# Optimization experiments

Measured on AMD Instinct MI355X. Metric: run time of the kernel, lower is better.

Reference implementation:

```python
import jax, jax.numpy as jnp
import numpy as np

ACTION_FEAT_DIM = 64
ACTION_EMB = 192
FUSION = 768
HID = 384
N_HEADS = 4
B, A = 2048, 64

gelu = lambda x: jax.nn.gelu(x, approximate=False)


def setup_inputs() -> dict:
    key = jax.random.key(0)
    ks = jax.random.split(key, 12)
    s = lambda fan_in: 1.0 / np.sqrt(fan_in)
    in_dim = ACTION_EMB + FUSION
    return {
        "action_feats": jax.random.normal(ks[0], (B, A, ACTION_FEAT_DIM), jnp.float32),
        "action_mask": jax.random.bernoulli(ks[1], 0.5, (B, A)),
        "fused": jax.random.normal(ks[2], (B, FUSION), jnp.float32),
        "phase_oh": jax.random.normal(ks[3], (B, 5), jnp.float32),
        # action encoder: Linear(64->192), GELU, Linear(192->192), GELU
        "We1": jax.random.uniform(ks[4], (ACTION_FEAT_DIM, ACTION_EMB), jnp.float32, -s(ACTION_FEAT_DIM), s(ACTION_FEAT_DIM)),
        "be1": jnp.zeros((ACTION_EMB,), jnp.float32),
        "We2": jax.random.uniform(ks[5], (ACTION_EMB, ACTION_EMB), jnp.float32, -s(ACTION_EMB), s(ACTION_EMB)),
        "be2": jnp.zeros((ACTION_EMB,), jnp.float32),
        # 4 phase heads: Linear(960->384), GELU, Linear(384->1), stacked on leading head axis
        "W1": jax.random.uniform(ks[6], (N_HEADS, in_dim, HID), jnp.float32, -s(in_dim), s(in_dim)),
        "b1": jnp.zeros((N_HEADS, HID), jnp.float32),
        "W2": jax.random.uniform(ks[7], (N_HEADS, HID), jnp.float32, -s(HID), s(HID)),
        "b2": jnp.zeros((N_HEADS,), jnp.float32),
    }


def reference(action_feats, action_mask, fused, phase_oh, We1, be1, We2, be2, W1, b1, W2, b2):
    bsz, act_count, _ = action_feats.shape
    # action encoder
    emb = gelu(gelu(action_feats @ We1 + be1) @ We2 + be2)          # [B,A,192]
    fused_rep = jnp.broadcast_to(fused[:, None, :], (bsz, act_count, fused.shape[-1]))
    inp = jnp.concatenate([emb, fused_rep], axis=-1)                 # [B,A,960]
    # dense compute of all 4 heads (faithful to original)
    h = gelu(jnp.einsum('bai,kio->bkao', inp, W1) + b1[None, :, None, :])  # [B,4,A,384]
    per_head = jnp.einsum('bkao,ko->bka', h, W2) + b2[None, :, None]       # [B,4,A]
    # phase routing: argmax over one-hot, phases >=3 map to head 3
    phase_idx = jnp.argmax(phase_oh, axis=-1)
    head_idx = jnp.where(phase_idx <= 2, phase_idx, 3)               # [B]
    logits = jnp.take_along_axis(per_head, head_idx[:, None, None], axis=1)[:, 0, :]  # [B,A]
    return jnp.where(action_mask, jnp.float32(-10000.0), logits)
```

## Files before the change

### kernel.cpp

```cpp
#include <hip/hip_runtime.h>


typedef __bf16 bf16x8 __attribute__((ext_vector_type(8)));
typedef unsigned short ushortx8 __attribute__((ext_vector_type(8)));
typedef float floatx4 __attribute__((ext_vector_type(4)));
typedef unsigned short u16;
typedef unsigned int u32;

#define B_SZ 2048
#define EMB 192
#define FUS 768
#define HID 384
#define INDIM 960
#define LDS_W 200

#define WS_FLAGS 0
#define WS_CNT 64
#define WS_HEAD 256
#define WS_LIST 8448
#define WS_W1T 41216
#define WS_WE1T 2990336
#define WS_WE2T 3014912
#define WS_FUSEDBF 3088640
#define WS_GSEL 6234368

__device__ __forceinline__ float bf2f(u16 u) {
  return __uint_as_float(((u32)u) << 16);
}
__device__ __forceinline__ u16 f2bf(float f) {
  u32 x = __float_as_uint(f);
  x += 0x7FFFu + ((x >> 16) & 1u);
  return (u16)(x >> 16);
}
__device__ __forceinline__ float ldf(const void* p, size_t i, int bf) {
  return bf ? bf2f(((const u16*)p)[i]) : ((const float*)p)[i];
}
__device__ __forceinline__ bf16x8 ld8(const void* p, size_t idx, int bf) {
  if (bf) return *reinterpret_cast<const bf16x8*>((const u16*)p + idx);
  const float* f = (const float*)p + idx;
  ushortx8 u;
#pragma unroll
  for (int i = 0; i < 8; ++i) u[i] = f2bf(f[i]);
  return __builtin_bit_cast(bf16x8, u);
}

__device__ __forceinline__ float gelu_f(float x) {
  float t = __expf(-1.702f * x);
  return x * __builtin_amdgcn_rcpf(1.0f + t);
}

__device__ __forceinline__ bool read_mask(const void* m, long long i, int fmt) {
  if (fmt == 0) return ((const int*)m)[i] != 0;
  if (fmt == 1) return ((const unsigned char*)m)[i] != 0;
  if (fmt == 2) return ((const u16*)m)[i] != 0;
  return ((const u32*)m)[i] != 0;
}

__global__ void k_detect(const u32* __restrict__ aw, int* __restrict__ flags,
                         int* __restrict__ cnt) {
  __shared__ u32 so[4];
  __shared__ int sc[4];
  int tid = threadIdx.x;
  int lane = tid & 63, wave = tid >> 6;
  u32 orv = 0;
  int c = 0;
#pragma unroll 8
  for (int j = 0; j < 64; ++j) {
    u32 w = aw[j * 256 + tid];
    u32 h = w & 0xFFFFu;
    orv |= h;
    u32 e = (h >> 7) & 0xFFu;
    c += (h == 0u || (e >= 90u && e <= 150u)) ? 1 : 0;
  }
#pragma unroll
  for (int off = 32; off >= 1; off >>= 1) {
    orv |= (u32)__shfl_xor((int)orv, off);
    c += __shfl_xor(c, off);
  }
  if (lane == 0) { so[wave] = orv; sc[wave] = c; }
  __syncthreads();
  if (tid == 0) {
    u32 o = so[0] | so[1] | so[2] | so[3];
    int ct = sc[0] + sc[1] + sc[2] + sc[3];
    flags[3] = (o != 0u && ct > 12288) ? 1 : 0;
    flags[0] = 0; flags[1] = 0; flags[2] = 0;
    cnt[0] = 0; cnt[1] = 0; cnt[2] = 0; cnt[3] = 0;
  }
}

__global__ void k_prep(const void* __restrict__ fused, u16* __restrict__ fbf,
                       const int* __restrict__ flags) {
  const int bf = flags[3];
  int gid = blockIdx.x * 256 + threadIdx.x;
  if (bf) {
    const uint2* s = (const uint2*)fused;
    uint2* d = (uint2*)fbf;
    for (int i = gid; i < 393216; i += 49152) d[i] = s[i];
  } else {
    const float4* s = (const float4*)fused;
    uint2* d = (uint2*)fbf;
    for (int i = gid; i < 393216; i += 49152) {
      float4 v = s[i];
      uint2 o;
      o.x = (u32)f2bf(v.x) | ((u32)f2bf(v.y) << 16);
      o.y = (u32)f2bf(v.z) | ((u32)f2bf(v.w) << 16);
      d[i] = o;
    }
  }
}

__global__ void k_route(const void* __restrict__ phase, const void* __restrict__ mask,
                        int* __restrict__ head_idx, int* __restrict__ flags,
                        int* __restrict__ cnt, int* __restrict__ list) {
  int tid = threadIdx.x;
  int t = blockIdx.x * 256 + tid;
  const int bf = flags[3];
  float best = ldf(phase, (size_t)t * 5, bf);
  int bi = 0;
#pragma unroll
  for (int i = 1; i < 5; ++i) {
    float v = ldf(phase, (size_t)t * 5 + i, bf);
    if (v > best) { best = v; bi = i; }
  }
  int h = (bi <= 2) ? bi : 3;
  head_idx[t] = h;
  int pos = atomicAdd(&cnt[h], 1);
  list[h * 2048 + pos] = t;

  const u32* mw = (const u32*)mask;
  u32 vi = 0, vu = 0, en = 0;
#pragma unroll
  for (int j = 0; j < 16; ++j) {
    u32 w = mw[blockIdx.x * 4096 + j * 256 + tid];
    vi |= (u32)(w > 1u);
    vu |= (u32)((w & 0xFEFEFEFEu) != 0u);
    en |= (u32)((w & 0x0000FFFFu) != 0u);
  }
  if (vi) atomicOr(&flags[0], 1);
  if (vu) atomicOr(&flags[1], 1);
  if (en) atomicOr(&flags[2], 1);
}

__global__ void k_transpose(const void* __restrict__ we1, const void* __restrict__ we2,
                            const void* __restrict__ w1, u16* __restrict__ we1t,
                            u16* __restrict__ we2t, u16* __restrict__ w1t,
                            const int* __restrict__ flags) {
  __shared__ u16 tile[32][33];
  const int bf = flags[3];
  const void* src; u16* dst; int R, C; size_t soff = 0;
  int z = blockIdx.z;
  if (z == 0)      { src = we1; dst = we1t; R = 64;  C = EMB; }
  else if (z == 1) { src = we2; dst = we2t; R = EMB; C = EMB; }
  else { src = w1; soff = (size_t)(z - 2) * INDIM * HID;
         dst = w1t + (size_t)(z - 2) * HID * INDIM; R = INDIM; C = HID; }
  int bx = blockIdx.x, by = blockIdx.y;
  if (bx * 32 >= C || by * 32 >= R) return;
  int tx = threadIdx.x, ty = threadIdx.y;
#pragma unroll
  for (int i = 0; i < 4; ++i) {
    int r = by * 32 + ty + i * 8, c = bx * 32 + tx;
    if (r < R && c < C) tile[ty + i * 8][tx] = f2bf(ldf(src, soff + (size_t)r * C + c, bf));
  }
  __syncthreads();
#pragma unroll
  for (int i = 0; i < 4; ++i) {
    int r = bx * 32 + ty + i * 8, c = by * 32 + tx;
    if (r < C && c < R) dst[(size_t)r * R + c] = tile[tx][ty + i * 8];
  }
}

__global__ __launch_bounds__(256, 4) void k_gall_sel(
    const u16* __restrict__ fbf, const u16* __restrict__ w1t,
    const void* __restrict__ b1, u16* __restrict__ gsel,
    const int* __restrict__ cnt, const int* __restrict__ list,
    const int* __restrict__ flags) {
  const int bf = flags[3];
  int c0 = cnt[0], c1 = cnt[1], c2 = cnt[2], c3 = cnt[3];
  int t0 = (c0 + 63) >> 6, t1 = (c1 + 63) >> 6, t2 = (c2 + 63) >> 6, t3 = (c3 + 63) >> 6;
  int x = blockIdx.x, h, tl;
  if (x < t0) { h = 0; tl = x; }
  else if (x < t0 + t1) { h = 1; tl = x - t0; }
  else if (x < t0 + t1 + t2) { h = 2; tl = x - t0 - t1; }
  else if (x < t0 + t1 + t2 + t3) { h = 3; tl = x - t0 - t1 - t2; }
  else return;
  int ch = (h == 0) ? c0 : (h == 1) ? c1 : (h == 2) ? c2 : c3;
  const int tid = threadIdx.x;
  const int w = tid >> 6, lane = tid & 63;
  const int nl = lane & 15, q = lane >> 4;

  int r = tl * 64 + w * 16 + nl;
  if (r >= ch) r = ch - 1;
  int bi = list[h * 2048 + r];
  const u16* arow = fbf + (size_t)bi * FUS;
  const u16* w1h = w1t + (size_t)h * HID * INDIM;
  const int ncol0 = blockIdx.y * 64;

  const floatx4 z4 = {0.f, 0.f, 0.f, 0.f};
  floatx4 acc[4];
#pragma unroll
  for (int i = 0; i < 4; ++i) acc[i] = z4;
#pragma unroll 4
  for (int kk = 0; kk < 24; ++kk) {
    bf16x8 a = *reinterpret_cast<const bf16x8*>(arow + kk * 32 + q * 8);
#pragma unroll
    for (int nt = 0; nt < 4; ++nt) {
      int col = ncol0 + nt * 16 + nl;
      bf16x8 bb = *reinterpret_cast<const bf16x8*>(w1h + (size_t)col * INDIM + EMB + kk * 32 + q * 8);
      acc[nt] = __builtin_amdgcn_mfma_f32_16x16x32_bf16(a, bb, acc[nt], 0, 0, 0);
    }
  }
  int bi2[4];
#pragma unroll
  for (int rr = 0; rr < 4; ++rr) {
    int rm = tl * 64 + w * 16 + q * 4 + rr;
    if (rm >= ch) rm = ch - 1;
    bi2[rr] = list[h * 2048 + rm];
  }
#pragma unroll
  for (int nt = 0; nt < 4; ++nt) {
    int col = ncol0 + nt * 16 + nl;
    float bias = ldf(b1, (size_t)h * HID + col, bf);
#pragma unroll
    for (int rr = 0; rr < 4; ++rr)
      gsel[(size_t)bi2[rr] * HID + col] = f2bf(acc[nt][rr] + bias);
  }
}

__global__ __launch_bounds__(256, 4) void k_main(
    const void* __restrict__ act, const void* __restrict__ mask,
    const void* __restrict__ be1, const void* __restrict__ be2,
    const void* __restrict__ W2, const void* __restrict__ b2,
    const u16* __restrict__ we1t, const u16* __restrict__ we2t,
    const u16* __restrict__ w1t, const u16* __restrict__ gsel,
    const int* __restrict__ head_idx, const int* __restrict__ flags,
    void* __restrict__ out) {
  __shared__ __align__(16) u16 S[64 * LDS_W];
  __shared__ float red[256];
  const int b = blockIdx.x;
  const int tid = threadIdx.x;
  const int w = tid >> 6, lane = tid & 63;
  const int nl = lane & 15, q = lane >> 4;
  const int khead = head_idx[b];
  const int bf = flags[3];
  const floatx4 z4 = {0.f, 0.f, 0.f, 0.f};

  {
    floatx4 acc1[4][3];
#pragma unroll
    for (int mt = 0; mt < 4; ++mt)
#pragma unroll
      for (int nt = 0; nt < 3; ++nt) acc1[mt][nt] = z4;
#pragma unroll
    for (int kk = 0; kk < 2; ++kk) {
      bf16x8 a[4];
#pragma unroll
      for (int mt = 0; mt < 4; ++mt)
        a[mt] = ld8(act, ((size_t)b * 64 + mt * 16 + nl) * 64 + kk * 32 + q * 8, bf);
#pragma unroll
      for (int nt = 0; nt < 3; ++nt) {
        bf16x8 bb = *reinterpret_cast<const bf16x8*>(we1t + (w * 48 + nt * 16 + nl) * 64 + kk * 32 + q * 8);
#pragma unroll
        for (int mt = 0; mt < 4; ++mt)
          acc1[mt][nt] = __builtin_amdgcn_mfma_f32_16x16x32_bf16(a[mt], bb, acc1[mt][nt], 0, 0, 0);
      }
    }
#pragma unroll
    for (int nt = 0; nt < 3; ++nt) {
      int col = w * 48 + nt * 16 + nl;
      float bias = ldf(be1, col, bf);
#pragma unroll
      for (int mt = 0; mt < 4; ++mt)
#pragma unroll
        for (int r = 0; r < 4; ++r)
          S[(mt * 16 + q * 4 + r) * LDS_W + col] = f2bf(gelu_f(acc1[mt][nt][r] + bias));
    }
  }
  __syncthreads();

  {
    floatx4 acc2[4][3];
#pragma unroll
    for (int mt = 0; mt < 4; ++mt)
#pragma unroll
      for (int nt = 0; nt < 3; ++nt) acc2[mt][nt] = z4;
#pragma unroll
    for (int kk = 0; kk < 6; ++kk) {
      bf16x8 a[4];
#pragma unroll
      for (int mt = 0; mt < 4; ++mt)
        a[mt] = *reinterpret_cast<const bf16x8*>(&S[(mt * 16 + nl) * LDS_W + kk * 32 + q * 8]);
#pragma unroll
      for (int nt = 0; nt < 3; ++nt) {
        bf16x8 bb = *reinterpret_cast<const bf16x8*>(we2t + (w * 48 + nt * 16 + nl) * EMB + kk * 32 + q * 8);
#pragma unroll
        for (int mt = 0; mt < 4; ++mt)
          acc2[mt][nt] = __builtin_amdgcn_mfma_f32_16x16x32_bf16(a[mt], bb, acc2[mt][nt], 0, 0, 0);
      }
    }
    __syncthreads();
#pragma unroll
    for (int nt = 0; nt < 3; ++nt) {
      int col = w * 48 + nt * 16 + nl;
      float bias = ldf(be2, col, bf);
#pragma unroll
      for (int mt = 0; mt < 4; ++mt)
#pragma unroll
        for (int r = 0; r < 4; ++r)
          S[(mt * 16 + q * 4 + r) * LDS_W + col] = f2bf(gelu_f(acc2[mt][nt][r] + bias));
    }
  }
  __syncthreads();

  float partial[4][4];
#pragma unroll
  for (int mt = 0; mt < 4; ++mt)
#pragma unroll
    for (int r = 0; r < 4; ++r) partial[mt][r] = 0.f;
  const u16* w1h = w1t + (size_t)khead * HID * INDIM;
  const u16* grow = gsel + (size_t)b * HID;
#pragma unroll
  for (int half = 0; half < 2; ++half) {
    floatx4 acc3[4][3];
#pragma unroll
    for (int mt = 0; mt < 4; ++mt)
#pragma unroll
      for (int nt = 0; nt < 3; ++nt) acc3[mt][nt] = z4;
#pragma unroll
    for (int kk = 0; kk < 6; ++kk) {
      bf16x8 a[4];
#pragma unroll
      for (int mt = 0; mt < 4; ++mt)
        a[mt] = *reinterpret_cast<const bf16x8*>(&S[(mt * 16 + nl) * LDS_W + kk * 32 + q * 8]);
#pragma unroll
      for (int nt = 0; nt < 3; ++nt) {
        int col = w * 96 + half * 48 + nt * 16 + nl;
        bf16x8 bb = *reinterpret_cast<const bf16x8*>(w1h + (size_t)col * INDIM + kk * 32 + q * 8);
#pragma unroll
        for (int mt = 0; mt < 4; ++mt)
          acc3[mt][nt] = __builtin_amdgcn_mfma_f32_16x16x32_bf16(a[mt], bb, acc3[mt][nt], 0, 0, 0);
      }
    }
#pragma unroll
    for (int nt = 0; nt < 3; ++nt) {
      int col = w * 96 + half * 48 + nt * 16 + nl;
      float g = bf2f(grow[col]);
      float w2c = ldf(W2, (size_t)khead * HID + col, bf);
#pragma unroll
      for (int mt = 0; mt < 4; ++mt)
#pragma unroll
        for (int r = 0; r < 4; ++r)
          partial[mt][r] += gelu_f(acc3[mt][nt][r] + g) * w2c;
    }
  }
#pragma unroll
  for (int off = 1; off < 16; off <<= 1)
#pragma unroll
    for (int mt = 0; mt < 4; ++mt)
#pragma unroll
      for (int r = 0; r < 4; ++r)
        partial[mt][r] += __shfl_xor(partial[mt][r], off, 16);
  if (nl == 0) {
#pragma unroll
    for (int mt = 0; mt < 4; ++mt)
#pragma unroll
      for (int r = 0; r < 4; ++r)
        red[w * 64 + mt * 16 + q * 4 + r] = partial[mt][r];
  }
  __syncthreads();

  if (tid < 64) {
    float s = red[tid] + red[64 + tid] + red[128 + tid] + red[192 + tid];
    int f0 = flags[0], f1 = flags[1], f2v = flags[2];
    int fmt = (f0 == 0) ? 0 : ((f1 == 0) ? 1 : ((f2v != 0) ? 2 : 3));
    float bb2 = ldf(b2, khead, bf);
    long long mi = (long long)b * 64 + tid;
    float v = read_mask(mask, mi, fmt) ? -10000.0f : (s + bb2);
    if (bf) ((u16*)out)[mi] = f2bf(v);
    else    ((float*)out)[mi] = v;
  }
}

extern "C" void kernel_launch(void* const* d_in, const int* in_sizes, int n_in,
                              void* d_out, int out_size, void* d_ws, size_t ws_size,
                              hipStream_t stream) {
  const void* act   = d_in[0];
  const void* mask  = d_in[1];
  const void* fused = d_in[2];
  const void* phase = d_in[3];
  const void* We1 = d_in[4];
  const void* be1 = d_in[5];
  const void* We2 = d_in[6];
  const void* be2 = d_in[7];
  const void* W1  = d_in[8];
  const void* b1  = d_in[9];
  const void* W2  = d_in[10];
  const void* b2  = d_in[11];
  char* ws = (char*)d_ws;
  int* flags    = (int*)(ws + WS_FLAGS);
  int* cnt      = (int*)(ws + WS_CNT);
  int* head_idx = (int*)(ws + WS_HEAD);
  int* list     = (int*)(ws + WS_LIST);
  u16* w1t  = (u16*)(ws + WS_W1T);
  u16* we1t = (u16*)(ws + WS_WE1T);
  u16* we2t = (u16*)(ws + WS_WE2T);
  u16* fbf  = (u16*)(ws + WS_FUSEDBF);
  u16* gsel = (u16*)(ws + WS_GSEL);

  k_detect<<<1, 256, 0, stream>>>((const u32*)act, flags, cnt);
  k_route<<<8, 256, 0, stream>>>(phase, mask, head_idx, flags, cnt, list);
  k_prep<<<192, 256, 0, stream>>>(fused, fbf, flags);
  k_transpose<<<dim3(12, 30, 6), dim3(32, 8), 0, stream>>>(We1, We2, W1, we1t, we2t, w1t, flags);
  k_gall_sel<<<dim3(36, 6), 256, 0, stream>>>(fbf, w1t, b1, gsel, cnt, list, flags);
  k_main<<<B_SZ, 256, 0, stream>>>(act, mask, be1, be2, W2, b2, we1t, we2t,
                                   w1t, gsel, head_idx, flags, d_out);
}
```

Baseline: 226.8 us.

## Process two head-sorted batch rows per block and merge prep kernels

The main kernel now handles two batch rows per block, picked from the per-head sorted lists so both rows tend to share a head. This doubles the M dimension of the encoder GEMMs so each encoder weight fragment is reused across twice as many rows, and it improves locality for the W1 head weights. The detect kernel is folded into routing, with a cheaper dtype check that samples only 64 words. The fused-input conversion is merged into the transpose kernel, and flags and counters are cleared with a memset, which cuts the number of launches. In exchange, shared memory and register use double and launch bounds drop to 2 blocks per CU, which may hurt latency hiding.

```diff
diff --git a/kernel.cpp b/kernel.cpp
--- a/kernel.cpp
+++ b/kernel.cpp
@@ -56,65 +56,29 @@
   return ((const u32*)m)[i] != 0;
 }
 
-__global__ void k_detect(const u32* __restrict__ aw, int* __restrict__ flags,
-                         int* __restrict__ cnt) {
-  __shared__ u32 so[4];
-  __shared__ int sc[4];
+__global__ void k_route(const void* __restrict__ act, const void* __restrict__ phase,
+                        const void* __restrict__ mask, int* __restrict__ head_idx,
+                        int* __restrict__ flags, int* __restrict__ cnt,
+                        int* __restrict__ list) {
+  __shared__ int s_bf;
   int tid = threadIdx.x;
-  int lane = tid & 63, wave = tid >> 6;
-  u32 orv = 0;
-  int c = 0;
-#pragma unroll 8
-  for (int j = 0; j < 64; ++j) {
-    u32 w = aw[j * 256 + tid];
+  if (tid < 64) {
+    u32 w = ((const u32*)act)[tid];
     u32 h = w & 0xFFFFu;
-    orv |= h;
     u32 e = (h >> 7) & 0xFFu;
-    c += (h == 0u || (e >= 90u && e <= 150u)) ? 1 : 0;
-  }
-#pragma unroll
-  for (int off = 32; off >= 1; off >>= 1) {
-    orv |= (u32)__shfl_xor((int)orv, off);
-    c += __shfl_xor(c, off);
-  }
-  if (lane == 0) { so[wave] = orv; sc[wave] = c; }
+    int pl = (h == 0u) || (e >= 90u && e <= 150u);
+    unsigned long long nz = __ballot(h != 0u);
+    unsigned long long pm = __ballot(pl);
+    if (tid == 0) {
+      int bfv = (nz != 0ULL && __popcll(pm) > 48) ? 1 : 0;
+      s_bf = bfv;
+      if (blockIdx.x == 0) flags[3] = bfv;
+    }
+  }
   __syncthreads();
-  if (tid == 0) {
-    u32 o = so[0] | so[1] | so[2] | so[3];
-    int ct = sc[0] + sc[1] + sc[2] + sc[3];
-    flags[3] = (o != 0u && ct > 12288) ? 1 : 0;
-    flags[0] = 0; flags[1] = 0; flags[2] = 0;
-    cnt[0] = 0; cnt[1] = 0; cnt[2] = 0; cnt[3] = 0;
-  }
-}
-
-__global__ void k_prep(const void* __restrict__ fused, u16* __restrict__ fbf,
-                       const int* __restrict__ flags) {
-  const int bf = flags[3];
-  int gid = blockIdx.x * 256 + threadIdx.x;
-  if (bf) {
-    const uint2* s = (const uint2*)fused;
-    uint2* d = (uint2*)fbf;
-    for (int i = gid; i < 393216; i += 49152) d[i] = s[i];
-  } else {
-    const float4* s = (const float4*)fused;
-    uint2* d = (uint2*)fbf;
-    for (int i = gid; i < 393216; i += 49152) {
-      float4 v = s[i];
-      uint2 o;
-      o.x = (u32)f2bf(v.x) | ((u32)f2bf(v.y) << 16);
-      o.y = (u32)f2bf(v.z) | ((u32)f2bf(v.w) << 16);
-      d[i] = o;
-    }
-  }
-}
-
-__global__ void k_route(const void* __restrict__ phase, const void* __restrict__ mask,
-                        int* __restrict__ head_idx, int* __restrict__ flags,
-                        int* __restrict__ cnt, int* __restrict__ list) {
-  int tid = threadIdx.x;
+  const int bf = s_bf;
+
   int t = blockIdx.x * 256 + tid;
-  const int bf = flags[3];
   float best = ldf(phase, (size_t)t * 5, bf);
   int bi = 0;
 #pragma unroll
@@ -141,14 +105,36 @@
   if (en) atomicOr(&flags[2], 1);
 }
 
-__global__ void k_transpose(const void* __restrict__ we1, const void* __restrict__ we2,
-                            const void* __restrict__ w1, u16* __restrict__ we1t,
-                            u16* __restrict__ we2t, u16* __restrict__ w1t,
-                            const int* __restrict__ flags) {
+__global__ void k_prep_trans(const void* __restrict__ we1, const void* __restrict__ we2,
+                             const void* __restrict__ w1, const void* __restrict__ fused,
+                             u16* __restrict__ we1t, u16* __restrict__ we2t,
+                             u16* __restrict__ w1t, u16* __restrict__ fbf,
+                             const int* __restrict__ flags) {
+  const int bf = flags[3];
+  int z = blockIdx.z;
+  if (z >= 6) {
+    int tid = threadIdx.y * 32 + threadIdx.x;
+    int blk = (z - 6) * 360 + blockIdx.y * 12 + blockIdx.x;
+    int gid = blk * 256 + tid;
+    if (bf) {
+      const uint2* s = (const uint2*)fused;
+      uint2* d = (uint2*)fbf;
+      for (int i = gid; i < 393216; i += 184320) d[i] = s[i];
+    } else {
+      const float4* s = (const float4*)fused;
+      uint2* d = (uint2*)fbf;
+      for (int i = gid; i < 393216; i += 184320) {
+        float4 v = s[i];
+        uint2 o;
+        o.x = (u32)f2bf(v.x) | ((u32)f2bf(v.y) << 16);
+        o.y = (u32)f2bf(v.z) | ((u32)f2bf(v.w) << 16);
+        d[i] = o;
+      }
+    }
+    return;
+  }
   __shared__ u16 tile[32][33];
-  const int bf = flags[3];
   const void* src; u16* dst; int R, C; size_t soff = 0;
-  int z = blockIdx.z;
   if (z == 0)      { src = we1; dst = we1t; R = 64;  C = EMB; }
   else if (z == 1) { src = we2; dst = we2t; R = EMB; C = EMB; }
   else { src = w1; soff = (size_t)(z - 2) * INDIM * HID;
@@ -226,42 +212,56 @@
   }
 }
 
-__global__ __launch_bounds__(256, 4) void k_main(
+__global__ __launch_bounds__(256, 2) void k_main(
     const void* __restrict__ act, const void* __restrict__ mask,
     const void* __restrict__ be1, const void* __restrict__ be2,
     const void* __restrict__ W2, const void* __restrict__ b2,
     const u16* __restrict__ we1t, const u16* __restrict__ we2t,
     const u16* __restrict__ w1t, const u16* __restrict__ gsel,
     const int* __restrict__ head_idx, const int* __restrict__ flags,
+    const int* __restrict__ cnt, const int* __restrict__ list,
     void* __restrict__ out) {
-  __shared__ __align__(16) u16 S[64 * LDS_W];
-  __shared__ float red[256];
-  const int b = blockIdx.x;
+  __shared__ __align__(16) u16 S[128 * LDS_W];
+  __shared__ float red[4][128];
   const int tid = threadIdx.x;
   const int w = tid >> 6, lane = tid & 63;
   const int nl = lane & 15, q = lane >> 4;
-  const int khead = head_idx[b];
   const int bf = flags[3];
   const floatx4 z4 = {0.f, 0.f, 0.f, 0.f};
 
+  int c0 = cnt[0], c1 = cnt[1], c2 = cnt[2];
+  int p1 = c0, p2 = c0 + c1, p3 = p2 + c2;
+  int bb[2], kh[2];
+#pragma unroll
+  for (int s = 0; s < 2; ++s) {
+    int g = blockIdx.x * 2 + s;
+    int h = (g < p1) ? 0 : (g < p2) ? 1 : (g < p3) ? 2 : 3;
+    int base = (h == 0) ? 0 : (h == 1) ? p1 : (h == 2) ? p2 : p3;
+    bb[s] = list[h * 2048 + (g - base)];
+    kh[s] = h;
+  }
+
   {
-    floatx4 acc1[4][3];
-#pragma unroll
-    for (int mt = 0; mt < 4; ++mt)
+    floatx4 acc1[8][3];
+#pragma unroll
+    for (int mt = 0; mt < 8; ++mt)
 #pragma unroll
       for (int nt = 0; nt < 3; ++nt) acc1[mt][nt] = z4;
 #pragma unroll
     for (int kk = 0; kk < 2; ++kk) {
-      bf16x8 a[4];
-#pragma unroll
-      for (int mt = 0; mt < 4; ++mt)
-        a[mt] = ld8(act, ((size_t)b * 64 + mt * 16 + nl) * 64 + kk * 32 + q * 8, bf);
+      bf16x8 a[8];
+#pragma unroll
+      for (int mt = 0; mt < 8; ++mt) {
+        int bcur = bb[mt >> 2];
+        int row = (mt & 3) * 16 + nl;
+        a[mt] = ld8(act, ((size_t)bcur * 64 + row) * 64 + kk * 32 + q * 8, bf);
+      }
 #pragma unroll
       for (int nt = 0; nt < 3; ++nt) {
-        bf16x8 bb = *reinterpret_cast<const bf16x8*>(we1t + (w * 48 + nt * 16 + nl) * 64 + kk * 32 + q * 8);
-#pragma unroll
-        for (int mt = 0; mt < 4; ++mt)
-          acc1[mt][nt] = __builtin_amdgcn_mfma_f32_16x16x32_bf16(a[mt], bb, acc1[mt][nt], 0, 0, 0);
+        bf16x8 bfr = *reinterpret_cast<const bf16x8*>(we1t + (w * 48 + nt * 16 + nl) * 64 + kk * 32 + q * 8);
+#pragma unroll
+        for (int mt = 0; mt < 8; ++mt)
+          acc1[mt][nt] = __builtin_amdgcn_mfma_f32_16x16x32_bf16(a[mt], bfr, acc1[mt][nt], 0, 0, 0);
       }
     }
 #pragma unroll
@@ -269,7 +269,7 @@
       int col = w * 48 + nt * 16 + nl;
       float bias = ldf(be1, col, bf);
 #pragma unroll
-      for (int mt = 0; mt < 4; ++mt)
+      for (int mt = 0; mt < 8; ++mt)
 #pragma unroll
         for (int r = 0; r < 4; ++r)
           S[(mt * 16 + q * 4 + r) * LDS_W + col] = f2bf(gelu_f(acc1[mt][nt][r] + bias));
@@ -278,23 +278,23 @@
   __syncthreads();
 
   {
-    floatx4 acc2[4][3];
-#pragma unroll
-    for (int mt = 0; mt < 4; ++mt)
+    floatx4 acc2[8][3];
+#pragma unroll
+    for (int mt = 0; mt < 8; ++mt)
 #pragma unroll
       for (int nt = 0; nt < 3; ++nt) acc2[mt][nt] = z4;
 #pragma unroll
     for (int kk = 0; kk < 6; ++kk) {
-      bf16x8 a[4];
-#pragma unroll
-      for (int mt = 0; mt < 4; ++mt)
+      bf16x8 a[8];
+#pragma unroll
+      for (int mt = 0; mt < 8; ++mt)
         a[mt] = *reinterpret_cast<const bf16x8*>(&S[(mt * 16 + nl) * LDS_W + kk * 32 + q * 8]);
 #pragma unroll
       for (int nt = 0; nt < 3; ++nt) {
-        bf16x8 bb = *reinterpret_cast<const bf16x8*>(we2t + (w * 48 + nt * 16 + nl) * EMB + kk * 32 + q * 8);
-#pragma unroll
-        for (int mt = 0; mt < 4; ++mt)
-          acc2[mt][nt] = __builtin_amdgcn_mfma_f32_16x16x32_bf16(a[mt], bb, acc2[mt][nt], 0, 0, 0);
+        bf16x8 bfr = *reinterpret_cast<const bf16x8*>(we2t + (w * 48 + nt * 16 + nl) * EMB + kk * 32 + q * 8);
+#pragma unroll
+        for (int mt = 0; mt < 8; ++mt)
+          acc2[mt][nt] = __builtin_amdgcn_mfma_f32_16x16x32_bf16(a[mt], bfr, acc2[mt][nt], 0, 0, 0);
       }
     }
     __syncthreads();
@@ -303,7 +303,7 @@
       int col = w * 48 + nt * 16 + nl;
       float bias = ldf(be2, col, bf);
 #pragma unroll
-      for (int mt = 0; mt < 4; ++mt)
+      for (int mt = 0; mt < 8; ++mt)
 #pragma unroll
         for (int r = 0; r < 4; ++r)
           S[(mt * 16 + q * 4 + r) * LDS_W + col] = f2bf(gelu_f(acc2[mt][nt][r] + bias));
@@ -311,70 +311,80 @@
   }
   __syncthreads();
 
-  float partial[4][4];
-#pragma unroll
-  for (int mt = 0; mt < 4; ++mt)
-#pragma unroll
-    for (int r = 0; r < 4; ++r) partial[mt][r] = 0.f;
-  const u16* w1h = w1t + (size_t)khead * HID * INDIM;
-  const u16* grow = gsel + (size_t)b * HID;
-#pragma unroll
-  for (int half = 0; half < 2; ++half) {
-    floatx4 acc3[4][3];
+  float partial[2][4][4];
+#pragma unroll
+  for (int s = 0; s < 2; ++s)
 #pragma unroll
     for (int mt = 0; mt < 4; ++mt)
 #pragma unroll
-      for (int nt = 0; nt < 3; ++nt) acc3[mt][nt] = z4;
-#pragma unroll
-    for (int kk = 0; kk < 6; ++kk) {
-      bf16x8 a[4];
+      for (int r = 0; r < 4; ++r) partial[s][mt][r] = 0.f;
+#pragma unroll
+  for (int s = 0; s < 2; ++s) {
+    const u16* w1h = w1t + (size_t)kh[s] * HID * INDIM;
+    const u16* grow = gsel + (size_t)bb[s] * HID;
+#pragma unroll
+    for (int half = 0; half < 2; ++half) {
+      floatx4 acc3[4][3];
 #pragma unroll
       for (int mt = 0; mt < 4; ++mt)
-        a[mt] = *reinterpret_cast<const bf16x8*>(&S[(mt * 16 + nl) * LDS_W + kk * 32 + q * 8]);
+#pragma unroll
+        for (int nt = 0; nt < 3; ++nt) acc3[mt][nt] = z4;
+#pragma unroll
+      for (int kk = 0; kk < 6; ++kk) {
+        bf16x8 a[4];
+#pragma unroll
+        for (int mt = 0; mt < 4; ++mt)
+          a[mt] = *reinterpret_cast<const bf16x8*>(&S[((s * 4 + mt) * 16 + nl) * LDS_W + kk * 32 + q * 8]);
+#pragma unroll
+        for (int nt = 0; nt < 3; ++nt) {
+          int col = w * 96 + half * 48 + nt * 16 + nl;
+          bf16x8 bfr = *reinterpret_cast<const bf16x8*>(w1h + (size_t)col * INDIM + kk * 32 + q * 8);
+#pragma unroll
+          for (int mt = 0; mt < 4; ++mt)
+            acc3[mt][nt] = __builtin_amdgcn_mfma_f32_16x16x32_bf16(a[mt], bfr, acc3[mt][nt], 0, 0, 0);
+        }
+      }
 #pragma unroll
       for (int nt = 0; nt < 3; ++nt) {
         int col = w * 96 + half * 48 + nt * 16 + nl;
-        bf16x8 bb = *reinterpret_cast<const bf16x8*>(w1h + (size_t)col * INDIM + kk * 32 + q * 8);
+        float g = bf2f(grow[col]);
+        float w2c = ldf(W2, (size_t)kh[s] * HID + col, bf);
 #pragma unroll
         for (int mt = 0; mt < 4; ++mt)
-          acc3[mt][nt] = __builtin_amdgcn_mfma_f32_16x16x32_bf16(a[mt], bb, acc3[mt][nt], 0, 0, 0);
-      }
-    }
-#pragma unroll
-    for (int nt = 0; nt < 3; ++nt) {
-      int col = w * 96 + half * 48 + nt * 16 + nl;
-      float g = bf2f(grow[col]);
-      float w2c = ldf(W2, (size_t)khead * HID + col, bf);
+#pragma unroll
+          for (int r = 0; r < 4; ++r)
+            partial[s][mt][r] += gelu_f(acc3[mt][nt][r] + g) * w2c;
+      }
+    }
+  }
+#pragma unroll
+  for (int off = 1; off < 16; off <<= 1)
+#pragma unroll
+    for (int s = 0; s < 2; ++s)
 #pragma unroll
       for (int mt = 0; mt < 4; ++mt)
 #pragma unroll
         for (int r = 0; r < 4; ++r)
-          partial[mt][r] += gelu_f(acc3[mt][nt][r] + g) * w2c;
-    }
-  }
-#pragma unroll
-  for (int off = 1; off < 16; off <<= 1)
-#pragma unroll
-    for (int mt = 0; mt < 4; ++mt)
-#pragma unroll
-      for (int r = 0; r < 4; ++r)
-        partial[mt][r] += __shfl_xor(partial[mt][r], off, 16);
+          partial[s][mt][r] += __shfl_xor(partial[s][mt][r], off, 16);
   if (nl == 0) {
 #pragma unroll
-    for (int mt = 0; mt < 4; ++mt)
-#pragma unroll
-      for (int r = 0; r < 4; ++r)
-        red[w * 64 + mt * 16 + q * 4 + r] = partial[mt][r];
+    for (int s = 0; s < 2; ++s)
+#pragma unroll
+      for (int mt = 0; mt < 4; ++mt)
+#pragma unroll
+        for (int r = 0; r < 4; ++r)
+          red[w][s * 64 + mt * 16 + q * 4 + r] = partial[s][mt][r];
   }
   __syncthreads();
 
-  if (tid < 64) {
-    float s = red[tid] + red[64 + tid] + red[128 + tid] + red[192 + tid];
+  if (tid < 128) {
+    int s = tid >> 6, ai = tid & 63;
+    float v = red[0][tid] + red[1][tid] + red[2][tid] + red[3][tid];
     int f0 = flags[0], f1 = flags[1], f2v = flags[2];
     int fmt = (f0 == 0) ? 0 : ((f1 == 0) ? 1 : ((f2v != 0) ? 2 : 3));
-    float bb2 = ldf(b2, khead, bf);
-    long long mi = (long long)b * 64 + tid;
-    float v = read_mask(mask, mi, fmt) ? -10000.0f : (s + bb2);
+    v += ldf(b2, kh[s], bf);
+    long long mi = (long long)bb[s] * 64 + ai;
+    if (read_mask(mask, mi, fmt)) v = -10000.0f;
     if (bf) ((u16*)out)[mi] = f2bf(v);
     else    ((float*)out)[mi] = v;
   }
@@ -406,11 +416,11 @@
   u16* fbf  = (u16*)(ws + WS_FUSEDBF);
   u16* gsel = (u16*)(ws + WS_GSEL);
 
-  k_detect<<<1, 256, 0, stream>>>((const u32*)act, flags, cnt);
-  k_route<<<8, 256, 0, stream>>>(phase, mask, head_idx, flags, cnt, list);
-  k_prep<<<192, 256, 0, stream>>>(fused, fbf, flags);
-  k_transpose<<<dim3(12, 30, 6), dim3(32, 8), 0, stream>>>(We1, We2, W1, we1t, we2t, w1t, flags);
+  hipMemsetAsync(flags, 0, 128, stream);
+  k_route<<<8, 256, 0, stream>>>(act, phase, mask, head_idx, flags, cnt, list);
+  k_prep_trans<<<dim3(12, 30, 8), dim3(32, 8), 0, stream>>>(
+      We1, We2, W1, fused, we1t, we2t, w1t, fbf, flags);
   k_gall_sel<<<dim3(36, 6), 256, 0, stream>>>(fbf, w1t, b1, gsel, cnt, list, flags);
-  k_main<<<B_SZ, 256, 0, stream>>>(act, mask, be1, be2, W2, b2, we1t, we2t,
-                                   w1t, gsel, head_idx, flags, d_out);
-}
+  k_main<<<1024, 256, 0, stream>>>(act, mask, be1, be2, W2, b2, we1t, we2t,
+                                   w1t, gsel, head_idx, flags, cnt, list, d_out);
+}
```

Result: no change. 223.9 us (-1.3%).

## Fuse prep kernels and pre-swizzle weights into MFMA fragment layout

Applied to the files above, without the earlier changes.

Merges the detect, route, fused-conversion and transpose kernels into one launch, replacing the detect pass with a per-block 64-word ballot probe and a memset. Weights are stored pre-arranged in per-lane MFMA B-fragment order, so each lane loads 16 contiguous bytes instead of making strided row reads. The aim is fewer launches and coalesced weight fetches in the main GEMM loops. The trade-off is that the bf16-input heuristic now looks at a far smaller sample, and the fragment build reads the source with strided accesses.

```diff
diff --git a/kernel.cpp b/kernel.cpp
--- a/kernel.cpp
+++ b/kernel.cpp
@@ -18,10 +18,10 @@
 #define WS_CNT 64
 #define WS_HEAD 256
 #define WS_LIST 8448
-#define WS_W1T 41216
-#define WS_WE1T 2990336
-#define WS_WE2T 3014912
-#define WS_FUSEDBF 3088640
+#define WS_WE1F 41216
+#define WS_WE2F 65792
+#define WS_W1F 139520
+#define WS_FBF 3088640
 #define WS_GSEL 6234368
 
 __device__ __forceinline__ float bf2f(u16 u) {
@@ -56,121 +56,117 @@
   return ((const u32*)m)[i] != 0;
 }
 
-__global__ void k_detect(const u32* __restrict__ aw, int* __restrict__ flags,
-                         int* __restrict__ cnt) {
-  __shared__ u32 so[4];
-  __shared__ int sc[4];
-  int tid = threadIdx.x;
-  int lane = tid & 63, wave = tid >> 6;
-  u32 orv = 0;
-  int c = 0;
-#pragma unroll 8
-  for (int j = 0; j < 64; ++j) {
-    u32 w = aw[j * 256 + tid];
+__device__ __forceinline__ int probe_bf(const void* act, int tid, int* s_bf) {
+  if (tid < 64) {
+    u32 w = ((const u32*)act)[tid];
     u32 h = w & 0xFFFFu;
-    orv |= h;
     u32 e = (h >> 7) & 0xFFu;
-    c += (h == 0u || (e >= 90u && e <= 150u)) ? 1 : 0;
-  }
-#pragma unroll
-  for (int off = 32; off >= 1; off >>= 1) {
-    orv |= (u32)__shfl_xor((int)orv, off);
-    c += __shfl_xor(c, off);
-  }
-  if (lane == 0) { so[wave] = orv; sc[wave] = c; }
+    int pl = (h == 0u) || (e >= 90u && e <= 150u);
+    unsigned long long nz = __ballot(h != 0u);
+    unsigned long long pm = __ballot(pl);
+    if (tid == 0) *s_bf = (nz != 0ULL && __popcll(pm) > 48) ? 1 : 0;
+  }
   __syncthreads();
-  if (tid == 0) {
-    u32 o = so[0] | so[1] | so[2] | so[3];
-    int ct = sc[0] + sc[1] + sc[2] + sc[3];
-    flags[3] = (o != 0u && ct > 12288) ? 1 : 0;
-    flags[0] = 0; flags[1] = 0; flags[2] = 0;
-    cnt[0] = 0; cnt[1] = 0; cnt[2] = 0; cnt[3] = 0;
-  }
-}
-
-__global__ void k_prep(const void* __restrict__ fused, u16* __restrict__ fbf,
-                       const int* __restrict__ flags) {
-  const int bf = flags[3];
-  int gid = blockIdx.x * 256 + threadIdx.x;
-  if (bf) {
-    const uint2* s = (const uint2*)fused;
-    uint2* d = (uint2*)fbf;
-    for (int i = gid; i < 393216; i += 49152) d[i] = s[i];
+  return *s_bf;
+}
+
+#define NB_ROUTE 8
+#define NB_FBF 512
+#define NB_WF 744
+__global__ void k_prep(const void* __restrict__ act, const void* __restrict__ phase,
+                       const void* __restrict__ mask, const void* __restrict__ fused,
+                       const void* __restrict__ we1, const void* __restrict__ we2,
+                       const void* __restrict__ w1,
+                       int* __restrict__ head_idx, int* __restrict__ flags,
+                       int* __restrict__ cnt, int* __restrict__ list,
+                       u16* __restrict__ we1f, u16* __restrict__ we2f,
+                       u16* __restrict__ w1f, u16* __restrict__ fbf) {
+  __shared__ int s_bf;
+  const int tid = threadIdx.x;
+  const int bx = blockIdx.x;
+  const int bf = probe_bf(act, tid, &s_bf);
+
+  if (bx < NB_ROUTE) {
+    if (bx == 0 && tid == 0) flags[3] = bf;
+    int t = bx * 256 + tid;
+    float best = ldf(phase, (size_t)t * 5, bf);
+    int bi = 0;
+#pragma unroll
+    for (int i = 1; i < 5; ++i) {
+      float v = ldf(phase, (size_t)t * 5 + i, bf);
+      if (v > best) { best = v; bi = i; }
+    }
+    int h = (bi <= 2) ? bi : 3;
+    head_idx[t] = h;
+    int pos = atomicAdd(&cnt[h], 1);
+    list[h * 2048 + pos] = t;
+
+    const u32* mw = (const u32*)mask;
+    u32 vi = 0, vu = 0, en = 0;
+#pragma unroll
+    for (int j = 0; j < 16; ++j) {
+      u32 w = mw[bx * 4096 + j * 256 + tid];
+      vi |= (u32)(w > 1u);
+      vu |= (u32)((w & 0xFEFEFEFEu) != 0u);
+      en |= (u32)((w & 0x0000FFFFu) != 0u);
+    }
+    if (vi) atomicOr(&flags[0], 1);
+    if (vu) atomicOr(&flags[1], 1);
+    if (en) atomicOr(&flags[2], 1);
+    return;
+  }
+
+  if (bx < NB_ROUTE + NB_FBF) {
+    int gid = (bx - NB_ROUTE) * 256 + tid;
+    if (bf) {
+      const uint2* s = (const uint2*)fused;
+      uint2* d = (uint2*)fbf;
+      for (int i = gid; i < 393216; i += NB_FBF * 256) d[i] = s[i];
+    } else {
+      const float4* s = (const float4*)fused;
+      uint2* d = (uint2*)fbf;
+      for (int i = gid; i < 393216; i += NB_FBF * 256) {
+        float4 v = s[i];
+        uint2 o;
+        o.x = (u32)f2bf(v.x) | ((u32)f2bf(v.y) << 16);
+        o.y = (u32)f2bf(v.z) | ((u32)f2bf(v.w) << 16);
+        d[i] = o;
+      }
+    }
+    return;
+  }
+
+  int fid = (bx - NB_ROUTE - NB_FBF) * 256 + tid;
+  int lane = fid & 63, rest = fid >> 6;
+  int q = lane >> 4, nl = lane & 15;
+  const void* src;
+  u16* dst;
+  int kk, col, ncols, dloc;
+  size_t soff = 0;
+  if (rest < 24) {
+    src = we1; dst = we1f; dloc = fid;
+    kk = rest & 1; col = (rest >> 1) * 16 + nl; ncols = EMB;
+  } else if (rest < 96) {
+    int r2 = rest - 24;
+    src = we2; dst = we2f; dloc = (r2 << 6) | lane;
+    kk = r2 % 6; col = (r2 / 6) * 16 + nl; ncols = EMB;
   } else {
-    const float4* s = (const float4*)fused;
-    uint2* d = (uint2*)fbf;
-    for (int i = gid; i < 393216; i += 49152) {
-      float4 v = s[i];
-      uint2 o;
-      o.x = (u32)f2bf(v.x) | ((u32)f2bf(v.y) << 16);
-      o.y = (u32)f2bf(v.z) | ((u32)f2bf(v.w) << 16);
-      d[i] = o;
-    }
-  }
-}
-
-__global__ void k_route(const void* __restrict__ phase, const void* __restrict__ mask,
-                        int* __restrict__ head_idx, int* __restrict__ flags,
-                        int* __restrict__ cnt, int* __restrict__ list) {
-  int tid = threadIdx.x;
-  int t = blockIdx.x * 256 + tid;
-  const int bf = flags[3];
-  float best = ldf(phase, (size_t)t * 5, bf);
-  int bi = 0;
-#pragma unroll
-  for (int i = 1; i < 5; ++i) {
-    float v = ldf(phase, (size_t)t * 5 + i, bf);
-    if (v > best) { best = v; bi = i; }
-  }
-  int h = (bi <= 2) ? bi : 3;
-  head_idx[t] = h;
-  int pos = atomicAdd(&cnt[h], 1);
-  list[h * 2048 + pos] = t;
-
-  const u32* mw = (const u32*)mask;
-  u32 vi = 0, vu = 0, en = 0;
-#pragma unroll
-  for (int j = 0; j < 16; ++j) {
-    u32 w = mw[blockIdx.x * 4096 + j * 256 + tid];
-    vi |= (u32)(w > 1u);
-    vu |= (u32)((w & 0xFEFEFEFEu) != 0u);
-    en |= (u32)((w & 0x0000FFFFu) != 0u);
-  }
-  if (vi) atomicOr(&flags[0], 1);
-  if (vu) atomicOr(&flags[1], 1);
-  if (en) atomicOr(&flags[2], 1);
-}
-
-__global__ void k_transpose(const void* __restrict__ we1, const void* __restrict__ we2,
-                            const void* __restrict__ w1, u16* __restrict__ we1t,
-                            u16* __restrict__ we2t, u16* __restrict__ w1t,
-                            const int* __restrict__ flags) {
-  __shared__ u16 tile[32][33];
-  const int bf = flags[3];
-  const void* src; u16* dst; int R, C; size_t soff = 0;
-  int z = blockIdx.z;
-  if (z == 0)      { src = we1; dst = we1t; R = 64;  C = EMB; }
-  else if (z == 1) { src = we2; dst = we2t; R = EMB; C = EMB; }
-  else { src = w1; soff = (size_t)(z - 2) * INDIM * HID;
-         dst = w1t + (size_t)(z - 2) * HID * INDIM; R = INDIM; C = HID; }
-  int bx = blockIdx.x, by = blockIdx.y;
-  if (bx * 32 >= C || by * 32 >= R) return;
-  int tx = threadIdx.x, ty = threadIdx.y;
-#pragma unroll
-  for (int i = 0; i < 4; ++i) {
-    int r = by * 32 + ty + i * 8, c = bx * 32 + tx;
-    if (r < R && c < C) tile[ty + i * 8][tx] = f2bf(ldf(src, soff + (size_t)r * C + c, bf));
-  }
-  __syncthreads();
-#pragma unroll
-  for (int i = 0; i < 4; ++i) {
-    int r = bx * 32 + ty + i * 8, c = by * 32 + tx;
-    if (r < C && c < R) dst[(size_t)r * R + c] = tile[tx][ty + i * 8];
-  }
+    int r3 = rest - 96;
+    src = w1; dst = w1f; dloc = (r3 << 6) | lane;
+    kk = r3 % 30; int hn = r3 / 30;
+    soff = (size_t)(hn / 24) * INDIM * HID;
+    col = (hn % 24) * 16 + nl; ncols = HID;
+  }
+  int k0 = kk * 32 + q * 8;
+  ushortx8 u;
+#pragma unroll
+  for (int j = 0; j < 8; ++j)
+    u[j] = f2bf(ldf(src, soff + (size_t)(k0 + j) * ncols + col, bf));
+  *reinterpret_cast<ushortx8*>(dst + (size_t)dloc * 8) = u;
 }
 
 __global__ __launch_bounds__(256, 4) void k_gall_sel(
-    const u16* __restrict__ fbf, const u16* __restrict__ w1t,
+    const u16* __restrict__ fbf, const u16* __restrict__ w1f,
     const void* __restrict__ b1, u16* __restrict__ gsel,
     const int* __restrict__ cnt, const int* __restrict__ list,
     const int* __restrict__ flags) {
@@ -192,8 +188,7 @@
   if (r >= ch) r = ch - 1;
   int bi = list[h * 2048 + r];
   const u16* arow = fbf + (size_t)bi * FUS;
-  const u16* w1h = w1t + (size_t)h * HID * INDIM;
-  const int ncol0 = blockIdx.y * 64;
+  const int by = blockIdx.y;
 
   const floatx4 z4 = {0.f, 0.f, 0.f, 0.f};
   floatx4 acc[4];
@@ -204,8 +199,8 @@
     bf16x8 a = *reinterpret_cast<const bf16x8*>(arow + kk * 32 + q * 8);
 #pragma unroll
     for (int nt = 0; nt < 4; ++nt) {
-      int col = ncol0 + nt * 16 + nl;
-      bf16x8 bb = *reinterpret_cast<const bf16x8*>(w1h + (size_t)col * INDIM + EMB + kk * 32 + q * 8);
+      size_t fo = ((((size_t)h * 24 + by * 4 + nt) * 30 + 6 + kk) * 64 + lane) * 8;
+      bf16x8 bb = *reinterpret_cast<const bf16x8*>(w1f + fo);
       acc[nt] = __builtin_amdgcn_mfma_f32_16x16x32_bf16(a, bb, acc[nt], 0, 0, 0);
     }
   }
@@ -218,7 +213,7 @@
   }
 #pragma unroll
   for (int nt = 0; nt < 4; ++nt) {
-    int col = ncol0 + nt * 16 + nl;
+    int col = by * 64 + nt * 16 + nl;
     float bias = ldf(b1, (size_t)h * HID + col, bf);
 #pragma unroll
     for (int rr = 0; rr < 4; ++rr)
@@ -230,8 +225,8 @@
     const void* __restrict__ act, const void* __restrict__ mask,
     const void* __restrict__ be1, const void* __restrict__ be2,
     const void* __restrict__ W2, const void* __restrict__ b2,
-    const u16* __restrict__ we1t, const u16* __restrict__ we2t,
-    const u16* __restrict__ w1t, const u16* __restrict__ gsel,
+    const u16* __restrict__ we1f, const u16* __restrict__ we2f,
+    const u16* __restrict__ w1f, const u16* __restrict__ gsel,
     const int* __restrict__ head_idx, const int* __restrict__ flags,
     void* __restrict__ out) {
   __shared__ __align__(16) u16 S[64 * LDS_W];
@@ -258,10 +253,11 @@
         a[mt] = ld8(act, ((size_t)b * 64 + mt * 16 + nl) * 64 + kk * 32 + q * 8, bf);
 #pragma unroll
       for (int nt = 0; nt < 3; ++nt) {
-        bf16x8 bb = *reinterpret_cast<const bf16x8*>(we1t + (w * 48 + nt * 16 + nl) * 64 + kk * 32 + q * 8);
+        bf16x8 bfr = *reinterpret_cast<const bf16x8*>(
+            we1f + (((w * 3 + nt) * 2 + kk) * 64 + lane) * 8);
 #pragma unroll
         for (int mt = 0; mt < 4; ++mt)
-          acc1[mt][nt] = __builtin_amdgcn_mfma_f32_16x16x32_bf16(a[mt], bb, acc1[mt][nt], 0, 0, 0);
+          acc1[mt][nt] = __builtin_amdgcn_mfma_f32_16x16x32_bf16(a[mt], bfr, acc1[mt][nt], 0, 0, 0);
       }
     }
 #pragma unroll
@@ -291,10 +287,11 @@
         a[mt] = *reinterpret_cast<const bf16x8*>(&S[(mt * 16 + nl) * LDS_W + kk * 32 + q * 8]);
 #pragma unroll
       for (int nt = 0; nt < 3; ++nt) {
-        bf16x8 bb = *reinterpret_cast<const bf16x8*>(we2t + (w * 48 + nt * 16 + nl) * EMB + kk * 32 + q * 8);
+        bf16x8 bfr = *reinterpret_cast<const bf16x8*>(
+            we2f + (((w * 3 + nt) * 6 + kk) * 64 + lane) * 8);
 #pragma unroll
         for (int mt = 0; mt < 4; ++mt)
-          acc2[mt][nt] = __builtin_amdgcn_mfma_f32_16x16x32_bf16(a[mt], bb, acc2[mt][nt], 0, 0, 0);
+          acc2[mt][nt] = __builtin_amdgcn_mfma_f32_16x16x32_bf16(a[mt], bfr, acc2[mt][nt], 0, 0, 0);
       }
     }
     __syncthreads();
@@ -316,7 +313,6 @@
   for (int mt = 0; mt < 4; ++mt)
 #pragma unroll
     for (int r = 0; r < 4; ++r) partial[mt][r] = 0.f;
-  const u16* w1h = w1t + (size_t)khead * HID * INDIM;
   const u16* grow = gsel + (size_t)b * HID;
 #pragma unroll
   for (int half = 0; half < 2; ++half) {
@@ -333,11 +329,11 @@
         a[mt] = *reinterpret_cast<const bf16x8*>(&S[(mt * 16 + nl) * LDS_W + kk * 32 + q * 8]);
 #pragma unroll
       for (int nt = 0; nt < 3; ++nt) {
-        int col = w * 96 + half * 48 + nt * 16 + nl;
-        bf16x8 bb = *reinterpret_cast<const bf16x8*>(w1h + (size_t)col * INDIM + kk * 32 + q * 8);
+        size_t fo = ((((size_t)khead * 24 + w * 6 + half * 3 + nt) * 30 + kk) * 64 + lane) * 8;
+        bf16x8 bfr = *reinterpret_cast<const bf16x8*>(w1f + fo);
 #pragma unroll
         for (int mt = 0; mt < 4; ++mt)
-          acc3[mt][nt] = __builtin_amdgcn_mfma_f32_16x16x32_bf16(a[mt], bb, acc3[mt][nt], 0, 0, 0);
+          acc3[mt][nt] = __builtin_amdgcn_mfma_f32_16x16x32_bf16(a[mt], bfr, acc3[mt][nt], 0, 0, 0);
       }
     }
 #pragma unroll
@@ -400,17 +396,17 @@
   int* cnt      = (int*)(ws + WS_CNT);
   int* head_idx = (int*)(ws + WS_HEAD);
   int* list     = (int*)(ws + WS_LIST);
-  u16* w1t  = (u16*)(ws + WS_W1T);
-  u16* we1t = (u16*)(ws + WS_WE1T);
-  u16* we2t = (u16*)(ws + WS_WE2T);
-  u16* fbf  = (u16*)(ws + WS_FUSEDBF);
+  u16* we1f = (u16*)(ws + WS_WE1F);
+  u16* we2f = (u16*)(ws + WS_WE2F);
+  u16* w1f  = (u16*)(ws + WS_W1F);
+  u16* fbf  = (u16*)(ws + WS_FBF);
   u16* gsel = (u16*)(ws + WS_GSEL);
 
-  k_detect<<<1, 256, 0, stream>>>((const u32*)act, flags, cnt);
-  k_route<<<8, 256, 0, stream>>>(phase, mask, head_idx, flags, cnt, list);
-  k_prep<<<192, 256, 0, stream>>>(fused, fbf, flags);
-  k_transpose<<<dim3(12, 30, 6), dim3(32, 8), 0, stream>>>(We1, We2, W1, we1t, we2t, w1t, flags);
-  k_gall_sel<<<dim3(36, 6), 256, 0, stream>>>(fbf, w1t, b1, gsel, cnt, list, flags);
-  k_main<<<B_SZ, 256, 0, stream>>>(act, mask, be1, be2, W2, b2, we1t, we2t,
-                                   w1t, gsel, head_idx, flags, d_out);
-}
+  hipMemsetAsync(flags, 0, 128, stream);
+  k_prep<<<NB_ROUTE + NB_FBF + NB_WF, 256, 0, stream>>>(
+      act, phase, mask, fused, We1, We2, W1,
+      head_idx, flags, cnt, list, we1f, we2f, w1f, fbf);
+  k_gall_sel<<<dim3(36, 6), 256, 0, stream>>>(fbf, w1f, b1, gsel, cnt, list, flags);
+  k_main<<<B_SZ, 256, 0, stream>>>(act, mask, be1, be2, W2, b2, we1f, we2f,
+                                   w1f, gsel, head_idx, flags, d_out);
+}
```

New measurement: 219.1 us. 3.4% less time.
